# Kernel optimization log

Measured on AMD Instinct MI355X. Metric: run time of the kernel, lower is better.

Reference implementation:

```python
import jax, jax.numpy as jnp
import numpy as np

# conv hyperparams matching init_kwargs (kernel=3, stride=1, pad=1, dilation=1, dg=1)
KH = KW = 3
SH = SW = 1
PH = PW = 1
DH = DW = 1


def setup_inputs() -> dict:
    key = jax.random.key(0)
    k1, k2, k3 = jax.random.split(key, 3)
    N, C, H, W = 4, 64, 128, 128
    OC, KN = 64, KH * KW
    x = jax.random.normal(k1, (N, C, H, W), jnp.float32)
    # offset channels: deformable_groups * kernel_n * 2, ordered (y, x) per point
    offset = jax.random.normal(k2, (N, KN * 2, H, W), jnp.float32)
    weight = jax.random.normal(k3, (OC, C, KN), jnp.float32) * 0.05
    return {"x": x, "offset": offset, "weight": weight}


def _bilinear(img, ix, iy):
    # img: (C, H, W); ix, iy: (KN, OH, OW) pixel coords; align_corners=True, zeros padding
    H, W = img.shape[1], img.shape[2]
    x0 = jnp.floor(ix)
    y0 = jnp.floor(iy)
    x1 = x0 + 1.0
    y1 = y0 + 1.0
    wx1 = ix - x0
    wx0 = 1.0 - wx1
    wy1 = iy - y0
    wy0 = 1.0 - wy1

    def gather(xc, yc, w):
        xi = jnp.clip(xc, 0, W - 1).astype(jnp.int32)
        yi = jnp.clip(yc, 0, H - 1).astype(jnp.int32)
        m = ((xc >= 0) & (xc <= W - 1) & (yc >= 0) & (yc <= H - 1)).astype(img.dtype)
        return img[:, yi, xi] * (w * m)[None]  # (C, KN, OH, OW)

    return (gather(x0, y0, wx0 * wy0) + gather(x1, y0, wx1 * wy0)
            + gather(x0, y1, wx0 * wy1) + gather(x1, y1, wx1 * wy1))


def reference(x, offset, weight):
    N, C, H, W = x.shape
    KN = weight.shape[2]
    OH, OW = offset.shape[2], offset.shape[3]
    half_h = (H - 1) / 2.0
    half_w = (W - 1) / 2.0
    # base mesh in normalized [-1,1] coords (same for every kernel point, per source)
    ys = jnp.arange(OH, dtype=x.dtype) * SH - PH + ((KH - 1) // 2) * DH
    xs = jnp.arange(OW, dtype=x.dtype) * SW - PW + ((KW - 1) // 2) * DW
    base_gy = (ys - half_h) / half_h  # (OH,)
    base_gx = (xs - half_w) / half_w  # (OW,)
    off = offset.reshape(N, KN, 2, OH, OW)
    gy = base_gy[None, None, :, None] + off[:, :, 0] / half_h  # (N, KN, OH, OW)
    gx = base_gx[None, None, None, :] + off[:, :, 1] / half_w
    # back to pixel coords (align_corners=True)
    ix = (gx + 1.0) * half_w
    iy = (gy + 1.0) * half_h
    sampled = jax.vmap(_bilinear)(x, ix, iy)  # (N, C, KN, OH, OW)
    # weight (OC, C, KN) contracted over (C, KN); note: source forward never adds bias
    out = jnp.einsum('oik,nikhw->nohw', weight, sampled)
    return out
```

## Files before the change

kernel.cpp:

```cpp
#include <hip/hip_runtime.h>
#include <hip/hip_bf16.h>


#define NB 4
#define CI 64
#define HH 128
#define WW 128
#define OCH 64
#define KNN 9
#define HW (HH * WW)

typedef unsigned int u32;
typedef unsigned short u16;
typedef __attribute__((ext_vector_type(8))) short bf16x8;
typedef __attribute__((ext_vector_type(4))) float f32x4;

__device__ inline u16 f2bf(float f) {
    u32 u = __float_as_uint(f);
    return (u16)((u + 0x7fffu + ((u >> 16) & 1u)) >> 16);
}
__device__ inline u32 pk2(float lo, float hi) {
    return (u32)f2bf(lo) | ((u32)f2bf(hi) << 16);
}
__device__ inline float2 up2v(u32 u) {
    return float2{__uint_as_float(u << 16), __uint_as_float(u & 0xffff0000u)};
}
__device__ inline u32 pkrn(float2 s) {
    union { __hip_bfloat162 b; u32 u; } c;
    c.b = __float22bfloat162_rn(s);
    return c.u;
}

__global__ __launch_bounds__(256) void prep_kernel(const float* __restrict__ x,
                                                   const float* __restrict__ w,
                                                   u16* __restrict__ xT,
                                                   u16* __restrict__ wf) {
    __shared__ float T[64 * 68];
    const int tid = threadIdx.x;
    if (blockIdx.x < NB * 256) {
        const int n = blockIdx.x >> 8;
        const int hw0 = (blockIdx.x & 255) << 6;
#pragma unroll
        for (int jj = 0; jj < 4; jj++) {
            int c = (tid >> 4) + (jj << 4);
            int hwq = (tid & 15) << 2;
            float4 v = *(const float4*)&x[(((n << 6) + c) << 14) + hw0 + hwq];
            *(float4*)&T[c * 68 + hwq] = v;
        }
        __syncthreads();
        const int hw_l = tid >> 2;
        const int cb = (tid & 3) << 4;
        u32 ou[8];
#pragma unroll
        for (int k = 0; k < 8; k++) {
            ou[k] = pk2(T[(cb + 2 * k) * 68 + hw_l], T[(cb + 2 * k + 1) * 68 + hw_l]);
        }
        u16* dst = xT + ((size_t)((n << 14) + hw0 + hw_l) << 6) + cb;
        *(uint4*)dst = make_uint4(ou[0], ou[1], ou[2], ou[3]);
        *(uint4*)(dst + 8) = make_uint4(ou[4], ou[5], ou[6], ou[7]);
    } else {
        int i = (blockIdx.x - NB * 256) * 256 + tid;
        if (i < KNN * 2 * 4 * 64 * 8) {
            int j = i & 7, l = (i >> 3) & 63, strip = (i >> 9) & 3,
                chunk = (i >> 11) & 1, kn = i >> 12;
            int oc = strip * 16 + (l & 15);
            int c = chunk * 32 + ((l >> 4) & 3) * 8 + j;
            wf[i] = f2bf(w[(oc * CI + c) * KNN + kn]);
        }
    }
}

__global__ __launch_bounds__(256, 4) void dcn_main_kernel(const u16* __restrict__ xT,
                                                          const float* __restrict__ off,
                                                          const u16* __restrict__ wf,
                                                          float* __restrict__ out) {
    __shared__ __align__(16) u32 tile[240 * 32];
    const int tid = threadIdx.x;
    const int l = tid & 63;
    const int wv = tid >> 6;

    const int b = blockIdx.x;
    const int xcd = b & 7;
    const int n = xcd >> 1;
    const int patch = (b >> 3) + ((xcd & 1) << 7);
    const int py = (patch >> 3) << 2;
    const int px = (patch & 7) << 4;
    const int ty = min(max(py - 3, 0), HH - 10);
    const int tx = min(max(px - 4, 0), WW - 24);

    const u16* xTn = xT + ((size_t)n << 20);
    const float* offn = off + n * (2 * KNN * HW);

    if (tid < 240) {
        const int tr = (tid * 171) >> 12;
        const int tc = tid - tr * 24;
        const u16* src = xTn + ((((ty + tr) << 7) + (tx + tc)) << 6);
        u32* dst = &tile[tid << 5];
        const int sw = tid & 7;
#pragma unroll
        for (int j = 0; j < 8; j++) {
            *(uint4*)&dst[(j ^ sw) << 2] = *(const uint4*)(src + (j << 3));
        }
    }

    const int col = l & 15;
    const int oh = py + wv;
    const int ow = px + col;
    const int rr = (oh << 7) + ow;
    const int qc = l >> 4;
    const int cb = qc << 3;

    float offy[KNN], offx[KNN];
#pragma unroll
    for (int kn = 0; kn < KNN; kn++) {
        offy[kn] = offn[(2 * kn) * HW + rr];
        offx[kn] = offn[(2 * kn + 1) * HW + rr];
    }

    __syncthreads();

    const bf16x8* wfv = (const bf16x8*)wf;
    f32x4 acc[4] = {{0, 0, 0, 0}, {0, 0, 0, 0}, {0, 0, 0, 0}, {0, 0, 0, 0}};

#pragma unroll
    for (int kn = 0; kn < KNN; kn++) {
        float iy = (float)oh + offy[kn], ix = (float)ow + offx[kn];
        float y0f = floorf(iy), x0f = floorf(ix);
        float wy1 = iy - y0f, wy0 = 1.f - wy1;
        float wx1 = ix - x0f, wx0 = 1.f - wx1;
        float my0 = (y0f >= 0.f && y0f <= 127.f) ? 1.f : 0.f;
        float my1 = (y0f >= -1.f && y0f <= 126.f) ? 1.f : 0.f;
        float mx0 = (x0f >= 0.f && x0f <= 127.f) ? 1.f : 0.f;
        float mx1 = (x0f >= -1.f && x0f <= 126.f) ? 1.f : 0.f;
        float W0 = wy0 * wx0 * my0 * mx0, W1 = wy0 * wx1 * my0 * mx1;
        float W2 = wy1 * wx0 * my1 * mx0, W3 = wy1 * wx1 * my1 * mx1;
        int y0 = min(max((int)y0f, 0), 127), y1 = min(max((int)y0f + 1, 0), 127);
        int x0 = min(max((int)x0f, 0), 127), x1 = min(max((int)x0f + 1, 0), 127);

        const int dy0 = min(max(y0 - ty, 0), 9), dy1 = min(max(y1 - ty, 0), 9);
        const int dx0 = min(max(x0 - tx, 0), 23), dx1 = min(max(x1 - tx, 0), 23);
        const int P0 = dy0 * 24 + dx0, P1 = dy0 * 24 + dx1;
        const int P2 = dy1 * 24 + dx0, P3 = dy1 * 24 + dx1;
        const bool oot = (y0 < ty) | (y1 > ty + 9) | (x0 < tx) | (x1 > tx + 23);

        uint4 Q0a = *(const uint4*)&tile[(P0 << 5) + (((qc    ) ^ (P0 & 7)) << 2)];
        uint4 Q0b = *(const uint4*)&tile[(P0 << 5) + (((qc + 4) ^ (P0 & 7)) << 2)];
        uint4 Q1a = *(const uint4*)&tile[(P1 << 5) + (((qc    ) ^ (P1 & 7)) << 2)];
        uint4 Q1b = *(const uint4*)&tile[(P1 << 5) + (((qc + 4) ^ (P1 & 7)) << 2)];
        uint4 Q2a = *(const uint4*)&tile[(P2 << 5) + (((qc    ) ^ (P2 & 7)) << 2)];
        uint4 Q2b = *(const uint4*)&tile[(P2 << 5) + (((qc + 4) ^ (P2 & 7)) << 2)];
        uint4 Q3a = *(const uint4*)&tile[(P3 << 5) + (((qc    ) ^ (P3 & 7)) << 2)];
        uint4 Q3b = *(const uint4*)&tile[(P3 << 5) + (((qc + 4) ^ (P3 & 7)) << 2)];
        if (oot) {
            const int O0 = ((y0 << 7) + x0) << 6, O1 = ((y0 << 7) + x1) << 6;
            const int O2 = ((y1 << 7) + x0) << 6, O3 = ((y1 << 7) + x1) << 6;
            Q0a = *(const uint4*)(xTn + O0 + cb);
            Q0b = *(const uint4*)(xTn + O0 + cb + 32);
            Q1a = *(const uint4*)(xTn + O1 + cb);
            Q1b = *(const uint4*)(xTn + O1 + cb + 32);
            Q2a = *(const uint4*)(xTn + O2 + cb);
            Q2b = *(const uint4*)(xTn + O2 + cb + 32);
            Q3a = *(const uint4*)(xTn + O3 + cb);
            Q3b = *(const uint4*)(xTn + O3 + cb + 32);
        }

#pragma unroll
        for (int cc = 0; cc < 2; cc++) {
            const u32* c0 = (const u32*)(cc ? &Q0b : &Q0a);
            const u32* c1 = (const u32*)(cc ? &Q1b : &Q1a);
            const u32* c2 = (const u32*)(cc ? &Q2b : &Q2a);
            const u32* c3 = (const u32*)(cc ? &Q3b : &Q3a);
            union { u32 u[4]; bf16x8 v; } B;
#pragma unroll
            for (int k = 0; k < 4; k++) {
                float2 s = up2v(c0[k]);
                s.x *= W0; s.y *= W0;
                float2 t1 = up2v(c1[k]);
                s.x = fmaf(t1.x, W1, s.x); s.y = fmaf(t1.y, W1, s.y);
                float2 t2 = up2v(c2[k]);
                s.x = fmaf(t2.x, W2, s.x); s.y = fmaf(t2.y, W2, s.y);
                float2 t3 = up2v(c3[k]);
                s.x = fmaf(t3.x, W3, s.x); s.y = fmaf(t3.y, W3, s.y);
                B.u[k] = pkrn(s);
            }
#pragma unroll
            for (int s4 = 0; s4 < 4; s4++) {
                bf16x8 A = wfv[((((kn << 1) + cc) << 2) + s4) * 64 + l];
                acc[s4] = __builtin_amdgcn_mfma_f32_16x16x32_bf16(A, B.v, acc[s4], 0, 0, 0);
            }
        }
    }

    const int rq = l >> 4;
    float* op = out + ((size_t)(n * OCH) << 14);
#pragma unroll
    for (int s = 0; s < 4; s++) {
        const int ocb = (s << 4) + (rq << 2);
#pragma unroll
        for (int g = 0; g < 4; g++) {
            op[((ocb + g) << 14) + rr] = acc[s][g];
        }
    }
}

__global__ __launch_bounds__(256) void dcn_fallback_kernel(
    const float* __restrict__ x, const float* __restrict__ off,
    const float* __restrict__ w, float* __restrict__ out) {
    int p = blockIdx.x * blockDim.x + threadIdx.x;
    int n = p / HW, r = p % HW, oh = r / WW, ow = r % WW;
    float acc[OCH];
#pragma unroll
    for (int i = 0; i < OCH; i++) acc[i] = 0.f;
    const float* xn = x + n * (CI * HW);
    const float* offn = off + n * (2 * KNN * HW);
    for (int kn = 0; kn < KNN; kn++) {
        float iy = (float)oh + offn[(2 * kn) * HW + r];
        float ix = (float)ow + offn[(2 * kn + 1) * HW + r];
        float y0f = floorf(iy), x0f = floorf(ix);
        float wy1 = iy - y0f, wy0 = 1.f - wy1, wx1 = ix - x0f, wx0 = 1.f - wx1;
        float my0 = (y0f >= 0.f && y0f <= 127.f) ? 1.f : 0.f;
        float my1 = (y0f >= -1.f && y0f <= 126.f) ? 1.f : 0.f;
        float mx0 = (x0f >= 0.f && x0f <= 127.f) ? 1.f : 0.f;
        float mx1 = (x0f >= -1.f && x0f <= 126.f) ? 1.f : 0.f;
        float w00 = wy0 * wx0 * my0 * mx0, w01 = wy0 * wx1 * my0 * mx1;
        float w10 = wy1 * wx0 * my1 * mx0, w11 = wy1 * wx1 * my1 * mx1;
        int y0 = min(max((int)y0f, 0), 127), y1 = min(max((int)y0f + 1, 0), 127);
        int x0 = min(max((int)x0f, 0), 127), x1 = min(max((int)x0f + 1, 0), 127);
        int o00 = y0 * WW + x0, o01 = y0 * WW + x1, o10 = y1 * WW + x0, o11 = y1 * WW + x1;
        for (int c = 0; c < CI; c++) {
            const float* xc = xn + c * HW;
            float s = xc[o00] * w00 + xc[o01] * w01 + xc[o10] * w10 + xc[o11] * w11;
#pragma unroll
            for (int oc = 0; oc < OCH; oc++) acc[oc] += w[(oc * CI + c) * KNN + kn] * s;
        }
    }
    float* outp = out + n * (OCH * HW) + r;
#pragma unroll
    for (int oc = 0; oc < OCH; oc++) outp[oc * HW] = acc[oc];
}

extern "C" void kernel_launch(void* const* d_in, const int* in_sizes, int n_in,
                              void* d_out, int out_size, void* d_ws, size_t ws_size,
                              hipStream_t stream) {
    const float* x = (const float*)d_in[0];
    const float* off = (const float*)d_in[1];
    const float* w = (const float*)d_in[2];
    float* out = (float*)d_out;

    const size_t xT_elems = (size_t)NB * HW * CI;
    const size_t wf_elems = (size_t)KNN * 2 * 4 * 64 * 8;
    const size_t need = (xT_elems + wf_elems) * sizeof(u16);

    if (ws_size >= need) {
        u16* xT = (u16*)d_ws;
        u16* wfr = xT + xT_elems;
        const int wf_blocks = (int)((wf_elems + 255) / 256);
        prep_kernel<<<NB * 256 + wf_blocks, 256, 0, stream>>>(x, w, xT, wfr);
        dcn_main_kernel<<<NB * 256, 256, 0, stream>>>(xT, off, wfr, out);
    } else {
        dcn_fallback_kernel<<<(NB * HW) / 256, 256, 0, stream>>>(x, off, w, out);
    }
}
```

Before: 98.31 us.

## Fuse NCHW-to-NHWC bf16 transpose into main kernel tile load

```diff
diff --git a/kernel.cpp b/kernel.cpp
--- a/kernel.cpp
+++ b/kernel.cpp
@@ -31,46 +31,19 @@
     return c.u;
 }
 
-__global__ __launch_bounds__(256) void prep_kernel(const float* __restrict__ x,
-                                                   const float* __restrict__ w,
-                                                   u16* __restrict__ xT,
-                                                   u16* __restrict__ wf) {
-    __shared__ float T[64 * 68];
-    const int tid = threadIdx.x;
-    if (blockIdx.x < NB * 256) {
-        const int n = blockIdx.x >> 8;
-        const int hw0 = (blockIdx.x & 255) << 6;
-#pragma unroll
-        for (int jj = 0; jj < 4; jj++) {
-            int c = (tid >> 4) + (jj << 4);
-            int hwq = (tid & 15) << 2;
-            float4 v = *(const float4*)&x[(((n << 6) + c) << 14) + hw0 + hwq];
-            *(float4*)&T[c * 68 + hwq] = v;
-        }
-        __syncthreads();
-        const int hw_l = tid >> 2;
-        const int cb = (tid & 3) << 4;
-        u32 ou[8];
-#pragma unroll
-        for (int k = 0; k < 8; k++) {
-            ou[k] = pk2(T[(cb + 2 * k) * 68 + hw_l], T[(cb + 2 * k + 1) * 68 + hw_l]);
-        }
-        u16* dst = xT + ((size_t)((n << 14) + hw0 + hw_l) << 6) + cb;
-        *(uint4*)dst = make_uint4(ou[0], ou[1], ou[2], ou[3]);
-        *(uint4*)(dst + 8) = make_uint4(ou[4], ou[5], ou[6], ou[7]);
-    } else {
-        int i = (blockIdx.x - NB * 256) * 256 + tid;
-        if (i < KNN * 2 * 4 * 64 * 8) {
-            int j = i & 7, l = (i >> 3) & 63, strip = (i >> 9) & 3,
-                chunk = (i >> 11) & 1, kn = i >> 12;
-            int oc = strip * 16 + (l & 15);
-            int c = chunk * 32 + ((l >> 4) & 3) * 8 + j;
-            wf[i] = f2bf(w[(oc * CI + c) * KNN + kn]);
-        }
-    }
-}
-
-__global__ __launch_bounds__(256, 4) void dcn_main_kernel(const u16* __restrict__ xT,
+__global__ __launch_bounds__(256) void wf_prep_kernel(const float* __restrict__ w,
+                                                      u16* __restrict__ wf) {
+    int i = blockIdx.x * 256 + threadIdx.x;
+    if (i < KNN * 2 * 4 * 64 * 8) {
+        int j = i & 7, l = (i >> 3) & 63, strip = (i >> 9) & 3,
+            chunk = (i >> 11) & 1, kn = i >> 12;
+        int oc = strip * 16 + (l & 15);
+        int c = chunk * 32 + ((l >> 4) & 3) * 8 + j;
+        wf[i] = f2bf(w[(oc * CI + c) * KNN + kn]);
+    }
+}
+
+__global__ __launch_bounds__(256, 4) void dcn_main_kernel(const float* __restrict__ x,
                                                           const float* __restrict__ off,
                                                           const u16* __restrict__ wf,
                                                           float* __restrict__ out) {
@@ -88,18 +61,22 @@
     const int ty = min(max(py - 3, 0), HH - 10);
     const int tx = min(max(px - 4, 0), WW - 24);
 
-    const u16* xTn = xT + ((size_t)n << 20);
+    const float* xN = x + ((size_t)n << 20);
     const float* offn = off + n * (2 * KNN * HW);
 
     if (tid < 240) {
         const int tr = (tid * 171) >> 12;
         const int tc = tid - tr * 24;
-        const u16* src = xTn + ((((ty + tr) << 7) + (tx + tc)) << 6);
+        const float* src = xN + ((ty + tr) << 7) + (tx + tc);
         u32* dst = &tile[tid << 5];
         const int sw = tid & 7;
 #pragma unroll
-        for (int j = 0; j < 8; j++) {
-            *(uint4*)&dst[(j ^ sw) << 2] = *(const uint4*)(src + (j << 3));
+        for (int q = 0; q < 8; q++) {
+            u32 o0 = pk2(src[(q * 8 + 0) * HW], src[(q * 8 + 1) * HW]);
+            u32 o1 = pk2(src[(q * 8 + 2) * HW], src[(q * 8 + 3) * HW]);
+            u32 o2 = pk2(src[(q * 8 + 4) * HW], src[(q * 8 + 5) * HW]);
+            u32 o3 = pk2(src[(q * 8 + 6) * HW], src[(q * 8 + 7) * HW]);
+            *(uint4*)&dst[(q ^ sw) << 2] = make_uint4(o0, o1, o2, o3);
         }
     }
 
@@ -152,16 +129,33 @@
         uint4 Q3a = *(const uint4*)&tile[(P3 << 5) + (((qc    ) ^ (P3 & 7)) << 2)];
         uint4 Q3b = *(const uint4*)&tile[(P3 << 5) + (((qc + 4) ^ (P3 & 7)) << 2)];
         if (oot) {
-            const int O0 = ((y0 << 7) + x0) << 6, O1 = ((y0 << 7) + x1) << 6;
-            const int O2 = ((y1 << 7) + x0) << 6, O3 = ((y1 << 7) + x1) << 6;
-            Q0a = *(const uint4*)(xTn + O0 + cb);
-            Q0b = *(const uint4*)(xTn + O0 + cb + 32);
-            Q1a = *(const uint4*)(xTn + O1 + cb);
-            Q1b = *(const uint4*)(xTn + O1 + cb + 32);
-            Q2a = *(const uint4*)(xTn + O2 + cb);
-            Q2b = *(const uint4*)(xTn + O2 + cb + 32);
-            Q3a = *(const uint4*)(xTn + O3 + cb);
-            Q3b = *(const uint4*)(xTn + O3 + cb + 32);
+            const int O0 = (y0 << 7) + x0, O1 = (y0 << 7) + x1;
+            const int O2 = (y1 << 7) + x0, O3 = (y1 << 7) + x1;
+            const float* p;
+            p = xN + O0 + cb * HW;
+            Q0a = make_uint4(pk2(p[0], p[HW]), pk2(p[2 * HW], p[3 * HW]),
+                             pk2(p[4 * HW], p[5 * HW]), pk2(p[6 * HW], p[7 * HW]));
+            p += 32 * HW;
+            Q0b = make_uint4(pk2(p[0], p[HW]), pk2(p[2 * HW], p[3 * HW]),
+                             pk2(p[4 * HW], p[5 * HW]), pk2(p[6 * HW], p[7 * HW]));
+            p = xN + O1 + cb * HW;
+            Q1a = make_uint4(pk2(p[0], p[HW]), pk2(p[2 * HW], p[3 * HW]),
+                             pk2(p[4 * HW], p[5 * HW]), pk2(p[6 * HW], p[7 * HW]));
+            p += 32 * HW;
+            Q1b = make_uint4(pk2(p[0], p[HW]), pk2(p[2 * HW], p[3 * HW]),
+                             pk2(p[4 * HW], p[5 * HW]), pk2(p[6 * HW], p[7 * HW]));
+            p = xN + O2 + cb * HW;
+            Q2a = make_uint4(pk2(p[0], p[HW]), pk2(p[2 * HW], p[3 * HW]),
+                             pk2(p[4 * HW], p[5 * HW]), pk2(p[6 * HW], p[7 * HW]));
+            p += 32 * HW;
+            Q2b = make_uint4(pk2(p[0], p[HW]), pk2(p[2 * HW], p[3 * HW]),
+                             pk2(p[4 * HW], p[5 * HW]), pk2(p[6 * HW], p[7 * HW]));
+            p = xN + O3 + cb * HW;
+            Q3a = make_uint4(pk2(p[0], p[HW]), pk2(p[2 * HW], p[3 * HW]),
+                             pk2(p[4 * HW], p[5 * HW]), pk2(p[6 * HW], p[7 * HW]));
+            p += 32 * HW;
+            Q3b = make_uint4(pk2(p[0], p[HW]), pk2(p[2 * HW], p[3 * HW]),
+                             pk2(p[4 * HW], p[5 * HW]), pk2(p[6 * HW], p[7 * HW]));
         }
 
 #pragma unroll
@@ -247,16 +241,14 @@
     const float* w = (const float*)d_in[2];
     float* out = (float*)d_out;
 
-    const size_t xT_elems = (size_t)NB * HW * CI;
     const size_t wf_elems = (size_t)KNN * 2 * 4 * 64 * 8;
-    const size_t need = (xT_elems + wf_elems) * sizeof(u16);
+    const size_t need = wf_elems * sizeof(u16);
 
     if (ws_size >= need) {
-        u16* xT = (u16*)d_ws;
-        u16* wfr = xT + xT_elems;
+        u16* wfr = (u16*)d_ws;
         const int wf_blocks = (int)((wf_elems + 255) / 256);
-        prep_kernel<<<NB * 256 + wf_blocks, 256, 0, stream>>>(x, w, xT, wfr);
-        dcn_main_kernel<<<NB * 256, 256, 0, stream>>>(xT, off, wfr, out);
+        wf_prep_kernel<<<wf_blocks, 256, 0, stream>>>(w, wfr);
+        dcn_main_kernel<<<NB * 256, 256, 0, stream>>>(x, off, wfr, out);
     } else {
         dcn_fallback_kernel<<<(NB * HW) / 256, 256, 0, stream>>>(x, off, w, out);
     }
```

After: 97.08 us, median of 2. No clear change (-1.3%).
